# Kernel tuning notes

Measured on AMD Instinct MI355X. Metric: run time of the kernel, lower is better.

The kernel has to match this reference:

```python
import jax, jax.numpy as jnp
import numpy as np

N = 50000
E = 800000
IN_C, HID, LAT = 256, 128, 64


def setup_inputs() -> dict:
    key = jax.random.key(0)
    ks = jax.random.split(key, 8)
    x = jax.random.normal(ks[0], (N, IN_C), dtype=jnp.float32)
    edge_index = jax.random.randint(ks[1], (2, E), 0, N, dtype=jnp.int64)
    # Glorot-ish scaled weights (PyG GCNConv: Linear weight + separate bias)
    W1 = jax.random.normal(ks[2], (IN_C, HID), dtype=jnp.float32) / np.sqrt(IN_C)
    b1 = jnp.zeros((HID,), dtype=jnp.float32)
    Wmu = jax.random.normal(ks[3], (HID, LAT), dtype=jnp.float32) / np.sqrt(HID)
    bmu = jnp.zeros((LAT,), dtype=jnp.float32)
    Wlv = jax.random.normal(ks[4], (HID, LAT), dtype=jnp.float32) / np.sqrt(HID)
    blv = jnp.zeros((LAT,), dtype=jnp.float32)
    return {"x": x, "edge_index": edge_index, "W1": W1, "b1": b1,
            "Wmu": Wmu, "bmu": bmu, "Wlv": Wlv, "blv": blv}


def gcn_conv(x, edge_index, W, b):
    """PyG GCNConv: add self-loops, sym-normalize, transform, scatter-add."""
    n = x.shape[0]
    loop = jnp.arange(n, dtype=edge_index.dtype)
    row = jnp.concatenate([edge_index[0], loop])  # source
    col = jnp.concatenate([edge_index[1], loop])  # target
    deg = jax.ops.segment_sum(jnp.ones_like(col, dtype=x.dtype), col, num_segments=n)
    dinv = jax.lax.rsqrt(jnp.maximum(deg, 1e-12))  # deg >= 1 due to self-loops
    norm = dinv[row] * dinv[col]                   # [E+N]
    h = x @ W                                      # transform first (smaller width)
    msg = h[row] * norm[:, None]                   # [E+N, out] gathered messages
    out = jax.ops.segment_sum(msg, col, num_segments=n)
    return out + b


def reference(x, edge_index, W1, b1, Wmu, bmu, Wlv, blv):
    h = jax.nn.relu(gcn_conv(x, edge_index, W1, b1))
    # dropout p=0.0 -> identity
    mu = gcn_conv(h, edge_index, Wmu, bmu)
    logvar = gcn_conv(h, edge_index, Wlv, blv)
    return (mu, logvar)
```

## Files before the change

### kernel.cpp

```cpp
#include <hip/hip_runtime.h>
#include <stdint.h>

#define NN   50000
#define NE   800000
#define INC  256
#define HID  128
#define LAT  64

typedef unsigned short u16;
typedef short v8s __attribute__((ext_vector_type(8)));
typedef float v4f __attribute__((ext_vector_type(4)));

#define SLAB_OFF 0
#define OFFS_OFF 802816
#define W1P_OFF  881216
#define W2P_OFF  897600
#define G1_OFF   905792

#define NBIN        196
#define OFFS_STRIDE 200
#define NSLAB       784

#define G2_OFFU  8388608
#define C2_CNT   8388608
#define C2_DINV  8438608
#define C2_BKT   8488608

#define GB    782

__device__ __forceinline__ u16 f2b(float f) {
    union { float f; uint32_t i; } c; c.f = f;
    uint32_t r = c.i + 0x7FFF + ((c.i >> 16) & 1);
    return (u16)(r >> 16);
}
__device__ __forceinline__ float blo(unsigned u) { return __uint_as_float(u << 16); }
__device__ __forceinline__ float bhi(unsigned u) { return __uint_as_float(u & 0xffff0000u); }

__device__ void pack1_body(const float* __restrict__ W1, u16* __restrict__ W1P, int b) {
    int tg = b * 256 + threadIdx.x;
    int ks = tg >> 9, rem = tg & 511;
    int nt = rem >> 6, lane = rem & 63;
    int quad = lane >> 4, l15 = lane & 15;
    u16 o[8];
    #pragma unroll
    for (int j = 0; j < 8; j++)
        o[j] = f2b(W1[(long)(ks * 32 + quad * 8 + j) * HID + nt * 16 + l15]);
    *(ushort4*)(W1P + (long)tg * 8)     = make_ushort4(o[0], o[1], o[2], o[3]);
    *(ushort4*)(W1P + (long)tg * 8 + 4) = make_ushort4(o[4], o[5], o[6], o[7]);
}

__device__ void pack2_body(const float* __restrict__ Wmu, const float* __restrict__ Wlv,
                           u16* __restrict__ W2P, int b) {
    int tg = b * 256 + threadIdx.x;
    int ks = tg >> 9, rem = tg & 511;
    int nt = rem >> 6, lane = rem & 63;
    int quad = lane >> 4, l15 = lane & 15;
    const float* W = (nt < 4) ? Wmu : Wlv;
    int ntl = (nt < 4) ? nt : nt - 4;
    u16 o[8];
    #pragma unroll
    for (int j = 0; j < 8; j++)
        o[j] = f2b(W[(long)(ks * 32 + quad * 8 + j) * LAT + ntl * 16 + l15]);
    *(ushort4*)(W2P + (long)tg * 8)     = make_ushort4(o[0], o[1], o[2], o[3]);
    *(ushort4*)(W2P + (long)tg * 8 + 4) = make_ushort4(o[4], o[5], o[6], o[7]);
}

__global__ __launch_bounds__(256) void k_fusedA(unsigned* csr, const float* W1,
        const float* Wmu, const float* Wlv) {
    int b = blockIdx.x;
    if (b < 16) pack1_body(W1, (u16*)(csr + W1P_OFF), b);
    else pack2_body(Wmu, Wlv, (u16*)(csr + W2P_OFF), b - 16);
}

__device__ void gemm1_body(const float* __restrict__ xbuf,
        const unsigned* __restrict__ csr, u16* __restrict__ g1, int blk) {
    const u16* W1P = (const u16*)(csr + W1P_OFF);
    int tid = threadIdx.x;
    int lane = tid & 63, w = tid >> 6;
    int quad = lane >> 4, l15 = lane & 15;
    int m0 = blk * 64 + w * 16;
    int arow = m0 + l15;
    int arc = arow < NN ? arow : NN - 1;
    const float* ap = xbuf + (long)arc * INC + quad * 8;
    const v8s* bp = (const v8s*)W1P;
    v4f acc[8];
    #pragma unroll
    for (int t = 0; t < 8; t++) acc[t] = (v4f){0.f, 0.f, 0.f, 0.f};

    float4 A[16];
    #pragma unroll
    for (int ks = 0; ks < 8; ks++) {
        A[2 * ks]     = *(const float4*)(ap + ks * 32);
        A[2 * ks + 1] = *(const float4*)(ap + ks * 32 + 4);
    }
    #pragma unroll
    for (int ks = 0; ks < 8; ks++) {
        float4 a0 = A[2 * ks], a1 = A[2 * ks + 1];
        v8s af;
        af[0] = (short)f2b(a0.x); af[1] = (short)f2b(a0.y);
        af[2] = (short)f2b(a0.z); af[3] = (short)f2b(a0.w);
        af[4] = (short)f2b(a1.x); af[5] = (short)f2b(a1.y);
        af[6] = (short)f2b(a1.z); af[7] = (short)f2b(a1.w);
        #pragma unroll
        for (int t = 0; t < 8; t++) {
            v8s bf = bp[(ks * 8 + t) * 64 + lane];
            acc[t] = __builtin_amdgcn_mfma_f32_16x16x32_bf16(af, bf, acc[t], 0, 0, 0);
        }
    }
    #pragma unroll
    for (int r = 0; r < 4; r++) {
        int rr = m0 + quad * 4 + r;
        if (rr < NN) {
            u16* dst = g1 + (long)rr * HID + l15;
            #pragma unroll
            for (int t = 0; t < 8; t++) dst[t * 16] = f2b(acc[t][r]);
        }
    }
}

__device__ void part_body(const int* __restrict__ row, const int* __restrict__ col,
                          unsigned* __restrict__ csr, int id) {
    __shared__ int hist[256];
    __shared__ int scanbuf[256];
    __shared__ unsigned recs[1024];
    int tid = threadIdx.x;
    int base = id * 1024;
    hist[tid] = 0;
    __syncthreads();
    int v[4], u[4];
    #pragma unroll
    for (int i = 0; i < 4; i++) {
        int e = base + i * 256 + tid;
        if (e < NE) {
            v[i] = col[e]; u[i] = row[e];
            atomicAdd(&hist[v[i] >> 8], 1);
        } else v[i] = -1;
    }
    __syncthreads();
    int x = hist[tid];
    scanbuf[tid] = x;
    __syncthreads();
    for (int s = 1; s < 256; s <<= 1) {
        int y = (tid >= s) ? scanbuf[tid - s] : 0;
        __syncthreads();
        scanbuf[tid] += y;
        __syncthreads();
    }
    int excl = scanbuf[tid] - x;
    u16* offs = (u16*)(csr + OFFS_OFF) + (long)id * OFFS_STRIDE;
    if (tid <= NBIN) offs[tid] = (u16)excl;
    hist[tid] = excl;
    __syncthreads();
    #pragma unroll
    for (int i = 0; i < 4; i++) {
        if (v[i] >= 0) {
            int slot = atomicAdd(&hist[v[i] >> 8], 1);
            recs[slot] = (unsigned)u[i] | ((unsigned)(v[i] & 255) << 16);
        }
    }
    __syncthreads();
    unsigned* slab = csr + SLAB_OFF + (long)id * 1024;
    #pragma unroll
    for (int i = 0; i < 4; i++) slab[i * 256 + tid] = recs[i * 256 + tid];
}

__global__ __launch_bounds__(256) void k_fusedB(const float* __restrict__ xbuf,
        unsigned* __restrict__ csr, u16* __restrict__ g1,
        const int* __restrict__ row, const int* __restrict__ col) {
    int b = blockIdx.x;
    if (b < GB) gemm1_body(xbuf, csr, g1, b);
    part_body(row, col, csr, b);
}

__global__ __launch_bounds__(256) void k_merge(const unsigned* __restrict__ csr,
        unsigned* __restrict__ xb) {
    __shared__ int cnt_lds[256];
    __shared__ u16 bkt_lds[256 * 64];
    int tid = threadIdx.x;
    int bin = blockIdx.x;
    cnt_lds[tid] = 0;
    __syncthreads();
    const u16* offs = (const u16*)(csr + OFFS_OFF);
    const unsigned* slab = csr + SLAB_OFF;
    for (int s = tid; s < NSLAB; s += 256) {
        int st = offs[s * OFFS_STRIDE + bin];
        int en = offs[s * OFFS_STRIDE + bin + 1];
        for (int j = st; j < en; j++) {
            unsigned r = slab[s * 1024 + j];
            int vlo = (int)(r >> 16);
            int slot = atomicAdd(&cnt_lds[vlo], 1);
            if (slot < 64) bkt_lds[(vlo << 6) + slot] = (u16)(r & 0xffffu);
        }
    }
    __syncthreads();
    int* cnt2 = (int*)(xb + C2_CNT);
    float* dinv = (float*)(xb + C2_DINV);
    u16* bkt2 = (u16*)(xb + C2_BKT);
    int v0 = bin << 8;
    {
        int v = v0 + tid;
        if (v < NN) {
            int deg = cnt_lds[tid];
            int cn = deg < 64 ? deg : 64;
            cnt2[v] = cn;
            dinv[v] = rsqrtf((float)(deg + 1));
        }
    }
    const uint4* src = (const uint4*)bkt_lds;
    #pragma unroll
    for (int i = 0; i < 8; i++) {
        int idx = i * 256 + tid;
        int node = idx >> 3;
        if (v0 + node < NN)
            ((uint4*)(bkt2 + ((long)(v0 + node) << 6)))[idx & 7] = src[idx];
    }
}

#define ACC8(P, D, W) if (P) { \
    a0 += D * blo(W.x); a1 += D * bhi(W.x); a2 += D * blo(W.y); a3 += D * bhi(W.y); \
    a4 += D * blo(W.z); a5 += D * bhi(W.z); a6 += D * blo(W.w); a7 += D * bhi(W.w); }
#define RED(S) \
    a0 += __shfl_xor(a0, S); a1 += __shfl_xor(a1, S); a2 += __shfl_xor(a2, S); \
    a3 += __shfl_xor(a3, S); a4 += __shfl_xor(a4, S); a5 += __shfl_xor(a5, S); \
    a6 += __shfl_xor(a6, S); a7 += __shfl_xor(a7, S);

#define GATHER_LOOP(SRC) \
    for (int t = 0; t < cn; t += 32) { \
        int t0 = t + q, t1 = t0 + 4, t2 = t0 + 8,  t3 = t0 + 12, \
            t4 = t0 + 16, t5 = t0 + 20, t6 = t0 + 24, t7 = t0 + 28; \
        bool p0 = t0 < cn, p1 = t1 < cn, p2 = t2 < cn, p3 = t3 < cn, \
             p4 = t4 < cn, p5 = t5 < cn, p6 = t6 < cn, p7 = t7 < cn; \
        int u0 = __shfl(idx, t0), u1 = __shfl(idx, t1), u2 = __shfl(idx, t2), \
            u3 = __shfl(idx, t3), u4 = __shfl(idx, t4), u5 = __shfl(idx, t5), \
            u6 = __shfl(idx, t6), u7 = __shfl(idx, t7); \
        float d0 = __shfl(dvu, t0), d1 = __shfl(dvu, t1), d2 = __shfl(dvu, t2), \
              d3 = __shfl(dvu, t3), d4 = __shfl(dvu, t4), d5 = __shfl(dvu, t5), \
              d6 = __shfl(dvu, t6), d7 = __shfl(dvu, t7); \
        uint4 w0, w1, w2, w3, w4, w5, w6, w7; \
        if (p0) w0 = *(const uint4*)(SRC + (long)u0 * HID + c * 8); \
        if (p1) w1 = *(const uint4*)(SRC + (long)u1 * HID + c * 8); \
        if (p2) w2 = *(const uint4*)(SRC + (long)u2 * HID + c * 8); \
        if (p3) w3 = *(const uint4*)(SRC + (long)u3 * HID + c * 8); \
        if (p4) w4 = *(const uint4*)(SRC + (long)u4 * HID + c * 8); \
        if (p5) w5 = *(const uint4*)(SRC + (long)u5 * HID + c * 8); \
        if (p6) w6 = *(const uint4*)(SRC + (long)u6 * HID + c * 8); \
        if (p7) w7 = *(const uint4*)(SRC + (long)u7 * HID + c * 8); \
        ACC8(p0, d0, w0) \
        ACC8(p1, d1, w1) \
        ACC8(p2, d2, w2) \
        ACC8(p3, d3, w3) \
        ACC8(p4, d4, w4) \
        ACC8(p5, d5, w5) \
        ACC8(p6, d6, w6) \
        ACC8(p7, d7, w7) \
    }

__global__ __launch_bounds__(256) void k_gather1(const u16* __restrict__ g1,
        const unsigned* __restrict__ xb, const float* __restrict__ b1,
        u16* __restrict__ h) {
    int tid = threadIdx.x;
    int lane = tid & 63, w = tid >> 6;
    int v = blockIdx.x * 4 + w;
    int q = lane >> 4, c = lane & 15;
    const int* cnt2 = (const int*)(xb + C2_CNT);
    const float* dinv = (const float*)(xb + C2_DINV);
    const u16* bkt2 = (const u16*)(xb + C2_BKT);
    int cn = cnt2[v];
    float dvv = dinv[v];
    int idx = (lane < cn) ? (int)bkt2[(v << 6) + lane] : 0;
    float dvu = dinv[idx];
    float a0 = 0.f, a1 = 0.f, a2 = 0.f, a3 = 0.f, a4 = 0.f, a5 = 0.f, a6 = 0.f, a7 = 0.f;
    if (q == 0) {
        uint4 wv = *(const uint4*)(g1 + (long)v * HID + c * 8);
        a0 = dvv * blo(wv.x); a1 = dvv * bhi(wv.x); a2 = dvv * blo(wv.y); a3 = dvv * bhi(wv.y);
        a4 = dvv * blo(wv.z); a5 = dvv * bhi(wv.z); a6 = dvv * blo(wv.w); a7 = dvv * bhi(wv.w);
    }
    GATHER_LOOP(g1)
    RED(16)
    RED(32)
    if (q == 0) {
        int j = c * 8;
        float r[8] = {a0, a1, a2, a3, a4, a5, a6, a7};
        unsigned p[4];
        #pragma unroll
        for (int i = 0; i < 4; i++) {
            float x0 = dvv * r[2 * i]     + b1[j + 2 * i];
            float x1 = dvv * r[2 * i + 1] + b1[j + 2 * i + 1];
            x0 = x0 > 0.f ? x0 : 0.f;
            x1 = x1 > 0.f ? x1 : 0.f;
            p[i] = (unsigned)f2b(x0) | ((unsigned)f2b(x1) << 16);
        }
        uint4 o; o.x = p[0]; o.y = p[1]; o.z = p[2]; o.w = p[3];
        *(uint4*)(h + (long)v * HID + j) = o;
    }
}

__global__ __launch_bounds__(256) void k_gemm2(const u16* __restrict__ h,
        const unsigned* __restrict__ csr, u16* __restrict__ g2) {
    const u16* W2P = (const u16*)(csr + W2P_OFF);
    int tid = threadIdx.x;
    int lane = tid & 63, w = tid >> 6;
    int quad = lane >> 4, l15 = lane & 15;
    int m0 = blockIdx.x * 64 + w * 16;
    int arow = m0 + l15;
    int arc = arow < NN ? arow : NN - 1;
    const u16* ap = h + (long)arc * HID + quad * 8;
    const v8s* bp = (const v8s*)W2P;
    v4f acc[8];
    #pragma unroll
    for (int t = 0; t < 8; t++) acc[t] = (v4f){0.f, 0.f, 0.f, 0.f};

    v8s af[4];
    #pragma unroll
    for (int ks = 0; ks < 4; ks++) af[ks] = *(const v8s*)(ap + ks * 32);

    #pragma unroll
    for (int ks = 0; ks < 4; ks++) {
        #pragma unroll
        for (int t = 0; t < 8; t++) {
            v8s bf = bp[(ks * 8 + t) * 64 + lane];
            acc[t] = __builtin_amdgcn_mfma_f32_16x16x32_bf16(af[ks], bf, acc[t], 0, 0, 0);
        }
    }
    #pragma unroll
    for (int r = 0; r < 4; r++) {
        int rr = m0 + quad * 4 + r;
        if (rr < NN) {
            u16* dst = g2 + (long)rr * HID + l15;
            #pragma unroll
            for (int t = 0; t < 8; t++) dst[t * 16] = f2b(acc[t][r]);
        }
    }
}

__global__ __launch_bounds__(256) void k_gather2(const u16* __restrict__ g2,
        const unsigned* __restrict__ xb, const float* __restrict__ bmu,
        const float* __restrict__ blv, float* __restrict__ out) {
    int tid = threadIdx.x;
    int lane = tid & 63, w = tid >> 6;
    int v = blockIdx.x * 4 + w;
    int q = lane >> 4, c = lane & 15;
    const int* cnt2 = (const int*)(xb + C2_CNT);
    const float* dinv = (const float*)(xb + C2_DINV);
    const u16* bkt2 = (const u16*)(xb + C2_BKT);
    int cn = cnt2[v];
    float dvv = dinv[v];
    int idx = (lane < cn) ? (int)bkt2[(v << 6) + lane] : 0;
    float dvu = dinv[idx];
    float a0 = 0.f, a1 = 0.f, a2 = 0.f, a3 = 0.f, a4 = 0.f, a5 = 0.f, a6 = 0.f, a7 = 0.f;
    if (q == 0) {
        uint4 wv = *(const uint4*)(g2 + (long)v * HID + c * 8);
        a0 = dvv * blo(wv.x); a1 = dvv * bhi(wv.x); a2 = dvv * blo(wv.y); a3 = dvv * bhi(wv.y);
        a4 = dvv * blo(wv.z); a5 = dvv * bhi(wv.z); a6 = dvv * blo(wv.w); a7 = dvv * bhi(wv.w);
    }
    GATHER_LOOP(g2)
    RED(16)
    RED(32)
    if (q == 0) {
        float r[8] = {a0, a1, a2, a3, a4, a5, a6, a7};
        if (c < 8) {
            int j = c * 8;
            float4 o0 = make_float4(dvv * r[0] + bmu[j],     dvv * r[1] + bmu[j + 1],
                                    dvv * r[2] + bmu[j + 2], dvv * r[3] + bmu[j + 3]);
            float4 o1 = make_float4(dvv * r[4] + bmu[j + 4], dvv * r[5] + bmu[j + 5],
                                    dvv * r[6] + bmu[j + 6], dvv * r[7] + bmu[j + 7]);
            float* dst = out + (long)v * LAT + j;
            *(float4*)dst = o0;
            *(float4*)(dst + 4) = o1;
        } else {
            int j = c * 8 - 64;
            float4 o0 = make_float4(dvv * r[0] + blv[j],     dvv * r[1] + blv[j + 1],
                                    dvv * r[2] + blv[j + 2], dvv * r[3] + blv[j + 3]);
            float4 o1 = make_float4(dvv * r[4] + blv[j + 4], dvv * r[5] + blv[j + 5],
                                    dvv * r[6] + blv[j + 6], dvv * r[7] + blv[j + 7]);
            float* dst = out + (long)NN * LAT + (long)v * LAT + j;
            *(float4*)dst = o0;
            *(float4*)(dst + 4) = o1;
        }
    }
}

extern "C" void kernel_launch(void* const* d_in, const int* in_sizes, int n_in,
                              void* d_out, int out_size, void* d_ws, size_t ws_size,
                              hipStream_t stream) {
    float* xbuf = (float*)d_in[0];
    const int* ei  = (const int*)d_in[1];
    const float* W1  = (const float*)d_in[2];
    const float* b1  = (const float*)d_in[3];
    const float* Wmu = (const float*)d_in[4];
    const float* bmu = (const float*)d_in[5];
    const float* Wlv = (const float*)d_in[6];
    const float* blv = (const float*)d_in[7];
    const int* row = ei;
    const int* col = ei + NE;

    unsigned* csr = (unsigned*)d_out;
    u16* g1   = (u16*)(csr + G1_OFF);
    u16* hbuf = (u16*)xbuf;
    u16* g2   = (u16*)xbuf + G2_OFFU;
    unsigned* xb = (unsigned*)xbuf;

    k_fusedA<<<24, 256, 0, stream>>>(csr, W1, Wmu, Wlv);

    k_fusedB<<<NSLAB, 256, 0, stream>>>(xbuf, csr, g1, row, col);
    k_merge <<<NBIN, 256, 0, stream>>>(csr, xb);
    k_gather1<<<NN / 4, 256, 0, stream>>>(g1, xb, b1, hbuf);

    k_gemm2 <<<GB, 256, 0, stream>>>(hbuf, csr, g2);
    k_gather2<<<NN / 4, 256, 0, stream>>>(g2, xb, bmu, blv, (float*)d_out);
}
```

Measured before the change: 223.1 us.

## Split gather features into 32-column slabs and stage GEMM1 A tile in LDS

The g1, h and g2 intermediates move from row-major [N,128] to four column slabs of [N,32], and each gather kernel launches four times as many blocks, one feature slice per block. The aim is a smaller per-pass working set so neighbour rows gathered at random stay in cache. The cost is that every block reloads the neighbour index and degree data four times and issues narrower 4-byte loads. GEMM1 also converts its x tile to bf16 once into padded LDS before the MFMA loop, replacing the per-lane register staging.

```diff
diff --git a/kernel.cpp b/kernel.cpp
--- a/kernel.cpp
+++ b/kernel.cpp
@@ -27,6 +27,7 @@
 #define C2_BKT   8488608
 
 #define GB    782
+#define GPB   12500
 
 __device__ __forceinline__ u16 f2b(float f) {
     union { float f; uint32_t i; } c; c.f = f;
@@ -73,34 +74,31 @@
 }
 
 __device__ void gemm1_body(const float* __restrict__ xbuf,
-        const unsigned* __restrict__ csr, u16* __restrict__ g1, int blk) {
+        const unsigned* __restrict__ csr, u16* __restrict__ g1, int blk,
+        u16* __restrict__ As) {
     const u16* W1P = (const u16*)(csr + W1P_OFF);
     int tid = threadIdx.x;
+    int m0b = blk * 64;
+    #pragma unroll
+    for (int i = 0; i < 16; i++) {
+        int idx = i * 256 + tid;
+        int r = idx >> 6, c4 = idx & 63;
+        int gr = m0b + r; gr = gr < NN ? gr : NN - 1;
+        float4 a = *(const float4*)(xbuf + (long)gr * INC + c4 * 4);
+        *(ushort4*)(As + r * 264 + c4 * 4) =
+            make_ushort4(f2b(a.x), f2b(a.y), f2b(a.z), f2b(a.w));
+    }
+    __syncthreads();
     int lane = tid & 63, w = tid >> 6;
     int quad = lane >> 4, l15 = lane & 15;
-    int m0 = blk * 64 + w * 16;
-    int arow = m0 + l15;
-    int arc = arow < NN ? arow : NN - 1;
-    const float* ap = xbuf + (long)arc * INC + quad * 8;
+    int m0 = m0b + w * 16;
     const v8s* bp = (const v8s*)W1P;
     v4f acc[8];
     #pragma unroll
     for (int t = 0; t < 8; t++) acc[t] = (v4f){0.f, 0.f, 0.f, 0.f};
-
-    float4 A[16];
     #pragma unroll
     for (int ks = 0; ks < 8; ks++) {
-        A[2 * ks]     = *(const float4*)(ap + ks * 32);
-        A[2 * ks + 1] = *(const float4*)(ap + ks * 32 + 4);
-    }
-    #pragma unroll
-    for (int ks = 0; ks < 8; ks++) {
-        float4 a0 = A[2 * ks], a1 = A[2 * ks + 1];
-        v8s af;
-        af[0] = (short)f2b(a0.x); af[1] = (short)f2b(a0.y);
-        af[2] = (short)f2b(a0.z); af[3] = (short)f2b(a0.w);
-        af[4] = (short)f2b(a1.x); af[5] = (short)f2b(a1.y);
-        af[6] = (short)f2b(a1.z); af[7] = (short)f2b(a1.w);
+        v8s af = *(const v8s*)(As + (w * 16 + l15) * 264 + ks * 32 + quad * 8);
         #pragma unroll
         for (int t = 0; t < 8; t++) {
             v8s bf = bp[(ks * 8 + t) * 64 + lane];
@@ -111,18 +109,16 @@
     for (int r = 0; r < 4; r++) {
         int rr = m0 + quad * 4 + r;
         if (rr < NN) {
-            u16* dst = g1 + (long)rr * HID + l15;
             #pragma unroll
-            for (int t = 0; t < 8; t++) dst[t * 16] = f2b(acc[t][r]);
+            for (int t = 0; t < 8; t++)
+                g1[((long)(t >> 1) * NN + rr) * 32 + (t & 1) * 16 + l15] = f2b(acc[t][r]);
         }
     }
 }
 
 __device__ void part_body(const int* __restrict__ row, const int* __restrict__ col,
-                          unsigned* __restrict__ csr, int id) {
-    __shared__ int hist[256];
-    __shared__ int scanbuf[256];
-    __shared__ unsigned recs[1024];
+                          unsigned* __restrict__ csr, int id,
+                          int* hist, int* scanbuf, unsigned* recs) {
     int tid = threadIdx.x;
     int base = id * 1024;
     hist[tid] = 0;
@@ -167,9 +163,13 @@
 __global__ __launch_bounds__(256) void k_fusedB(const float* __restrict__ xbuf,
         unsigned* __restrict__ csr, u16* __restrict__ g1,
         const int* __restrict__ row, const int* __restrict__ col) {
+    __shared__ __align__(16) u16 As[64 * 264];
+    __shared__ int hist[256];
+    __shared__ int scanbuf[256];
+    __shared__ unsigned recs[1024];
     int b = blockIdx.x;
-    if (b < GB) gemm1_body(xbuf, csr, g1, b);
-    part_body(row, col, csr, b);
+    if (b < GB) gemm1_body(xbuf, csr, g1, b, As);
+    part_body(row, col, csr, b, hist, scanbuf, recs);
 }
 
 __global__ __launch_bounds__(256) void k_merge(const unsigned* __restrict__ csr,
@@ -216,15 +216,8 @@
     }
 }
 
-#define ACC8(P, D, W) if (P) { \
-    a0 += D * blo(W.x); a1 += D * bhi(W.x); a2 += D * blo(W.y); a3 += D * bhi(W.y); \
-    a4 += D * blo(W.z); a5 += D * bhi(W.z); a6 += D * blo(W.w); a7 += D * bhi(W.w); }
-#define RED(S) \
-    a0 += __shfl_xor(a0, S); a1 += __shfl_xor(a1, S); a2 += __shfl_xor(a2, S); \
-    a3 += __shfl_xor(a3, S); a4 += __shfl_xor(a4, S); a5 += __shfl_xor(a5, S); \
-    a6 += __shfl_xor(a6, S); a7 += __shfl_xor(a7, S);
-
-#define GATHER_LOOP(SRC) \
+#define GACC(P, D, W) if (P) { a0 += D * blo(W); a1 += D * bhi(W); }
+#define GATHER_SLICE_LOOP(GS) \
     for (int t = 0; t < cn; t += 32) { \
         int t0 = t + q, t1 = t0 + 4, t2 = t0 + 8,  t3 = t0 + 12, \
             t4 = t0 + 16, t5 = t0 + 20, t6 = t0 + 24, t7 = t0 + 28; \
@@ -236,31 +229,36 @@
         float d0 = __shfl(dvu, t0), d1 = __shfl(dvu, t1), d2 = __shfl(dvu, t2), \
               d3 = __shfl(dvu, t3), d4 = __shfl(dvu, t4), d5 = __shfl(dvu, t5), \
               d6 = __shfl(dvu, t6), d7 = __shfl(dvu, t7); \
-        uint4 w0, w1, w2, w3, w4, w5, w6, w7; \
-        if (p0) w0 = *(const uint4*)(SRC + (long)u0 * HID + c * 8); \
-        if (p1) w1 = *(const uint4*)(SRC + (long)u1 * HID + c * 8); \
-        if (p2) w2 = *(const uint4*)(SRC + (long)u2 * HID + c * 8); \
-        if (p3) w3 = *(const uint4*)(SRC + (long)u3 * HID + c * 8); \
-        if (p4) w4 = *(const uint4*)(SRC + (long)u4 * HID + c * 8); \
-        if (p5) w5 = *(const uint4*)(SRC + (long)u5 * HID + c * 8); \
-        if (p6) w6 = *(const uint4*)(SRC + (long)u6 * HID + c * 8); \
-        if (p7) w7 = *(const uint4*)(SRC + (long)u7 * HID + c * 8); \
-        ACC8(p0, d0, w0) \
-        ACC8(p1, d1, w1) \
-        ACC8(p2, d2, w2) \
-        ACC8(p3, d3, w3) \
-        ACC8(p4, d4, w4) \
-        ACC8(p5, d5, w5) \
-        ACC8(p6, d6, w6) \
-        ACC8(p7, d7, w7) \
-    }
+        unsigned w0 = 0, w1 = 0, w2 = 0, w3 = 0, w4 = 0, w5 = 0, w6 = 0, w7 = 0; \
+        if (p0) w0 = *(const unsigned*)(GS + (long)u0 * 32 + c * 2); \
+        if (p1) w1 = *(const unsigned*)(GS + (long)u1 * 32 + c * 2); \
+        if (p2) w2 = *(const unsigned*)(GS + (long)u2 * 32 + c * 2); \
+        if (p3) w3 = *(const unsigned*)(GS + (long)u3 * 32 + c * 2); \
+        if (p4) w4 = *(const unsigned*)(GS + (long)u4 * 32 + c * 2); \
+        if (p5) w5 = *(const unsigned*)(GS + (long)u5 * 32 + c * 2); \
+        if (p6) w6 = *(const unsigned*)(GS + (long)u6 * 32 + c * 2); \
+        if (p7) w7 = *(const unsigned*)(GS + (long)u7 * 32 + c * 2); \
+        GACC(p0, d0, w0) \
+        GACC(p1, d1, w1) \
+        GACC(p2, d2, w2) \
+        GACC(p3, d3, w3) \
+        GACC(p4, d4, w4) \
+        GACC(p5, d5, w5) \
+        GACC(p6, d6, w6) \
+        GACC(p7, d7, w7) \
+    }
+#define GRED() \
+    a0 += __shfl_xor(a0, 16); a1 += __shfl_xor(a1, 16); \
+    a0 += __shfl_xor(a0, 32); a1 += __shfl_xor(a1, 32);
 
 __global__ __launch_bounds__(256) void k_gather1(const u16* __restrict__ g1,
         const unsigned* __restrict__ xb, const float* __restrict__ b1,
         u16* __restrict__ h) {
     int tid = threadIdx.x;
     int lane = tid & 63, w = tid >> 6;
-    int v = blockIdx.x * 4 + w;
+    int bid = blockIdx.x;
+    int p = bid / GPB;
+    int v = (bid - p * GPB) * 4 + w;
     int q = lane >> 4, c = lane & 15;
     const int* cnt2 = (const int*)(xb + C2_CNT);
     const float* dinv = (const float*)(xb + C2_DINV);
@@ -269,29 +267,22 @@
     float dvv = dinv[v];
     int idx = (lane < cn) ? (int)bkt2[(v << 6) + lane] : 0;
     float dvu = dinv[idx];
-    float a0 = 0.f, a1 = 0.f, a2 = 0.f, a3 = 0.f, a4 = 0.f, a5 = 0.f, a6 = 0.f, a7 = 0.f;
+    const u16* gs = g1 + (long)p * NN * 32;
+    float a0 = 0.f, a1 = 0.f;
     if (q == 0) {
-        uint4 wv = *(const uint4*)(g1 + (long)v * HID + c * 8);
-        a0 = dvv * blo(wv.x); a1 = dvv * bhi(wv.x); a2 = dvv * blo(wv.y); a3 = dvv * bhi(wv.y);
-        a4 = dvv * blo(wv.z); a5 = dvv * bhi(wv.z); a6 = dvv * blo(wv.w); a7 = dvv * bhi(wv.w);
-    }
-    GATHER_LOOP(g1)
-    RED(16)
-    RED(32)
+        unsigned wv = *(const unsigned*)(gs + (long)v * 32 + c * 2);
+        a0 = dvv * blo(wv); a1 = dvv * bhi(wv);
+    }
+    GATHER_SLICE_LOOP(gs)
+    GRED()
     if (q == 0) {
-        int j = c * 8;
-        float r[8] = {a0, a1, a2, a3, a4, a5, a6, a7};
-        unsigned p[4];
-        #pragma unroll
-        for (int i = 0; i < 4; i++) {
-            float x0 = dvv * r[2 * i]     + b1[j + 2 * i];
-            float x1 = dvv * r[2 * i + 1] + b1[j + 2 * i + 1];
-            x0 = x0 > 0.f ? x0 : 0.f;
-            x1 = x1 > 0.f ? x1 : 0.f;
-            p[i] = (unsigned)f2b(x0) | ((unsigned)f2b(x1) << 16);
-        }
-        uint4 o; o.x = p[0]; o.y = p[1]; o.z = p[2]; o.w = p[3];
-        *(uint4*)(h + (long)v * HID + j) = o;
+        int j = p * 32 + c * 2;
+        float x0 = dvv * a0 + b1[j];
+        float x1 = dvv * a1 + b1[j + 1];
+        x0 = x0 > 0.f ? x0 : 0.f;
+        x1 = x1 > 0.f ? x1 : 0.f;
+        *(unsigned*)(h + ((long)p * NN + v) * 32 + c * 2) =
+            (unsigned)f2b(x0) | ((unsigned)f2b(x1) << 16);
     }
 }
 
@@ -304,7 +295,6 @@
     int m0 = blockIdx.x * 64 + w * 16;
     int arow = m0 + l15;
     int arc = arow < NN ? arow : NN - 1;
-    const u16* ap = h + (long)arc * HID + quad * 8;
     const v8s* bp = (const v8s*)W2P;
     v4f acc[8];
     #pragma unroll
@@ -312,7 +302,8 @@
 
     v8s af[4];
     #pragma unroll
-    for (int ks = 0; ks < 4; ks++) af[ks] = *(const v8s*)(ap + ks * 32);
+    for (int ks = 0; ks < 4; ks++)
+        af[ks] = *(const v8s*)(h + ((long)ks * NN + arc) * 32 + quad * 8);
 
     #pragma unroll
     for (int ks = 0; ks < 4; ks++) {
@@ -326,9 +317,9 @@
     for (int r = 0; r < 4; r++) {
         int rr = m0 + quad * 4 + r;
         if (rr < NN) {
-            u16* dst = g2 + (long)rr * HID + l15;
             #pragma unroll
-            for (int t = 0; t < 8; t++) dst[t * 16] = f2b(acc[t][r]);
+            for (int t = 0; t < 8; t++)
+                g2[((long)(t >> 1) * NN + rr) * 32 + (t & 1) * 16 + l15] = f2b(acc[t][r]);
         }
     }
 }
@@ -338,7 +329,9 @@
         const float* __restrict__ blv, float* __restrict__ out) {
     int tid = threadIdx.x;
     int lane = tid & 63, w = tid >> 6;
-    int v = blockIdx.x * 4 + w;
+    int bid = blockIdx.x;
+    int p = bid / GPB;
+    int v = (bid - p * GPB) * 4 + w;
     int q = lane >> 4, c = lane & 15;
     const int* cnt2 = (const int*)(xb + C2_CNT);
     const float* dinv = (const float*)(xb + C2_DINV);
@@ -347,35 +340,23 @@
     float dvv = dinv[v];
     int idx = (lane < cn) ? (int)bkt2[(v << 6) + lane] : 0;
     float dvu = dinv[idx];
-    float a0 = 0.f, a1 = 0.f, a2 = 0.f, a3 = 0.f, a4 = 0.f, a5 = 0.f, a6 = 0.f, a7 = 0.f;
+    const u16* gs = g2 + (long)p * NN * 32;
+    float a0 = 0.f, a1 = 0.f;
     if (q == 0) {
-        uint4 wv = *(const uint4*)(g2 + (long)v * HID + c * 8);
-        a0 = dvv * blo(wv.x); a1 = dvv * bhi(wv.x); a2 = dvv * blo(wv.y); a3 = dvv * bhi(wv.y);
-        a4 = dvv * blo(wv.z); a5 = dvv * bhi(wv.z); a6 = dvv * blo(wv.w); a7 = dvv * bhi(wv.w);
-    }
-    GATHER_LOOP(g2)
-    RED(16)
-    RED(32)
+        unsigned wv = *(const unsigned*)(gs + (long)v * 32 + c * 2);
+        a0 = dvv * blo(wv); a1 = dvv * bhi(wv);
+    }
+    GATHER_SLICE_LOOP(gs)
+    GRED()
     if (q == 0) {
-        float r[8] = {a0, a1, a2, a3, a4, a5, a6, a7};
-        if (c < 8) {
-            int j = c * 8;
-            float4 o0 = make_float4(dvv * r[0] + bmu[j],     dvv * r[1] + bmu[j + 1],
-                                    dvv * r[2] + bmu[j + 2], dvv * r[3] + bmu[j + 3]);
-            float4 o1 = make_float4(dvv * r[4] + bmu[j + 4], dvv * r[5] + bmu[j + 5],
-                                    dvv * r[6] + bmu[j + 6], dvv * r[7] + bmu[j + 7]);
-            float* dst = out + (long)v * LAT + j;
-            *(float4*)dst = o0;
-            *(float4*)(dst + 4) = o1;
+        int j = p * 32 + c * 2;
+        if (j < 64) {
+            *(float2*)(out + (long)v * LAT + j) =
+                make_float2(dvv * a0 + bmu[j], dvv * a1 + bmu[j + 1]);
         } else {
-            int j = c * 8 - 64;
-            float4 o0 = make_float4(dvv * r[0] + blv[j],     dvv * r[1] + blv[j + 1],
-                                    dvv * r[2] + blv[j + 2], dvv * r[3] + blv[j + 3]);
-            float4 o1 = make_float4(dvv * r[4] + blv[j + 4], dvv * r[5] + blv[j + 5],
-                                    dvv * r[6] + blv[j + 6], dvv * r[7] + blv[j + 7]);
-            float* dst = out + (long)NN * LAT + (long)v * LAT + j;
-            *(float4*)dst = o0;
-            *(float4*)(dst + 4) = o1;
+            int jl = j - 64;
+            *(float2*)(out + (long)NN * LAT + (long)v * LAT + jl) =
+                make_float2(dvv * a0 + blv[jl], dvv * a1 + blv[jl + 1]);
         }
     }
 }
@@ -404,8 +385,8 @@
 
     k_fusedB<<<NSLAB, 256, 0, stream>>>(xbuf, csr, g1, row, col);
     k_merge <<<NBIN, 256, 0, stream>>>(csr, xb);
-    k_gather1<<<NN / 4, 256, 0, stream>>>(g1, xb, b1, hbuf);
+    k_gather1<<<4 * GPB, 256, 0, stream>>>(g1, xb, b1, hbuf);
 
     k_gemm2 <<<GB, 256, 0, stream>>>(hbuf, csr, g2);
-    k_gather2<<<NN / 4, 256, 0, stream>>>(g2, xb, bmu, blv, (float*)d_out);
-}
+    k_gather2<<<4 * GPB, 256, 0, stream>>>(g2, xb, bmu, blv, (float*)d_out);
+}
```

Result: slower. 280.0 us (+25.5%).

## Fuse layer-1 gather with second GEMM via LDS and stage GEMM1 A tile in LDS

Applied to the files above, without the earlier changes.

Merges the layer-1 aggregation kernel with the second GEMM. Each 64-row block now aggregates its own nodes into an LDS tile of ReLU'd bf16 features and runs the MFMA transform straight from LDS, so the h round-trip through global memory and one launch go away. The first GEMM also now stages its A tile in padded LDS using coalesced float4 loads, instead of each lane loading strided rows itself. The trade-off is that the fused kernel runs only GB blocks, about 782, with each wave handling 16 nodes serially, so gather parallelism and latency hiding drop. The extra LDS in k_fusedB may also cut occupancy for the partition work.

```diff
diff --git a/kernel.cpp b/kernel.cpp
--- a/kernel.cpp
+++ b/kernel.cpp
@@ -73,34 +73,31 @@
 }
 
 __device__ void gemm1_body(const float* __restrict__ xbuf,
-        const unsigned* __restrict__ csr, u16* __restrict__ g1, int blk) {
+        const unsigned* __restrict__ csr, u16* __restrict__ g1, int blk,
+        u16* __restrict__ As) {
     const u16* W1P = (const u16*)(csr + W1P_OFF);
     int tid = threadIdx.x;
+    int m0b = blk * 64;
+    #pragma unroll
+    for (int i = 0; i < 16; i++) {
+        int idx = i * 256 + tid;
+        int r = idx >> 6, c4 = idx & 63;
+        int gr = m0b + r; gr = gr < NN ? gr : NN - 1;
+        float4 a = *(const float4*)(xbuf + (long)gr * INC + c4 * 4);
+        *(ushort4*)(As + r * 264 + c4 * 4) =
+            make_ushort4(f2b(a.x), f2b(a.y), f2b(a.z), f2b(a.w));
+    }
+    __syncthreads();
     int lane = tid & 63, w = tid >> 6;
     int quad = lane >> 4, l15 = lane & 15;
-    int m0 = blk * 64 + w * 16;
-    int arow = m0 + l15;
-    int arc = arow < NN ? arow : NN - 1;
-    const float* ap = xbuf + (long)arc * INC + quad * 8;
+    int m0 = m0b + w * 16;
     const v8s* bp = (const v8s*)W1P;
     v4f acc[8];
     #pragma unroll
     for (int t = 0; t < 8; t++) acc[t] = (v4f){0.f, 0.f, 0.f, 0.f};
-
-    float4 A[16];
     #pragma unroll
     for (int ks = 0; ks < 8; ks++) {
-        A[2 * ks]     = *(const float4*)(ap + ks * 32);
-        A[2 * ks + 1] = *(const float4*)(ap + ks * 32 + 4);
-    }
-    #pragma unroll
-    for (int ks = 0; ks < 8; ks++) {
-        float4 a0 = A[2 * ks], a1 = A[2 * ks + 1];
-        v8s af;
-        af[0] = (short)f2b(a0.x); af[1] = (short)f2b(a0.y);
-        af[2] = (short)f2b(a0.z); af[3] = (short)f2b(a0.w);
-        af[4] = (short)f2b(a1.x); af[5] = (short)f2b(a1.y);
-        af[6] = (short)f2b(a1.z); af[7] = (short)f2b(a1.w);
+        v8s af = *(const v8s*)(As + (w * 16 + l15) * 264 + ks * 32 + quad * 8);
         #pragma unroll
         for (int t = 0; t < 8; t++) {
             v8s bf = bp[(ks * 8 + t) * 64 + lane];
@@ -119,10 +116,8 @@
 }
 
 __device__ void part_body(const int* __restrict__ row, const int* __restrict__ col,
-                          unsigned* __restrict__ csr, int id) {
-    __shared__ int hist[256];
-    __shared__ int scanbuf[256];
-    __shared__ unsigned recs[1024];
+                          unsigned* __restrict__ csr, int id,
+                          int* hist, int* scanbuf, unsigned* recs) {
     int tid = threadIdx.x;
     int base = id * 1024;
     hist[tid] = 0;
@@ -167,9 +162,13 @@
 __global__ __launch_bounds__(256) void k_fusedB(const float* __restrict__ xbuf,
         unsigned* __restrict__ csr, u16* __restrict__ g1,
         const int* __restrict__ row, const int* __restrict__ col) {
+    __shared__ __align__(16) u16 As[64 * 264];
+    __shared__ int hist[256];
+    __shared__ int scanbuf[256];
+    __shared__ unsigned recs[1024];
     int b = blockIdx.x;
-    if (b < GB) gemm1_body(xbuf, csr, g1, b);
-    part_body(row, col, csr, b);
+    if (b < GB) gemm1_body(xbuf, csr, g1, b, As);
+    part_body(row, col, csr, b, hist, scanbuf, recs);
 }
 
 __global__ __launch_bounds__(256) void k_merge(const unsigned* __restrict__ csr,
@@ -223,7 +222,6 @@
     a0 += __shfl_xor(a0, S); a1 += __shfl_xor(a1, S); a2 += __shfl_xor(a2, S); \
     a3 += __shfl_xor(a3, S); a4 += __shfl_xor(a4, S); a5 += __shfl_xor(a5, S); \
     a6 += __shfl_xor(a6, S); a7 += __shfl_xor(a7, S);
-
 #define GATHER_LOOP(SRC) \
     for (int t = 0; t < cn; t += 32) { \
         int t0 = t + q, t1 = t0 + 4, t2 = t0 + 8,  t3 = t0 + 12, \
@@ -255,71 +253,73 @@
         ACC8(p7, d7, w7) \
     }
 
-__global__ __launch_bounds__(256) void k_gather1(const u16* __restrict__ g1,
+#define HPAD 136
+__global__ __launch_bounds__(256) void k_fusedD(const u16* __restrict__ g1,
         const unsigned* __restrict__ xb, const float* __restrict__ b1,
-        u16* __restrict__ h) {
+        const unsigned* __restrict__ csr, u16* __restrict__ g2) {
+    __shared__ __align__(16) u16 hs[64 * HPAD];
     int tid = threadIdx.x;
     int lane = tid & 63, w = tid >> 6;
-    int v = blockIdx.x * 4 + w;
     int q = lane >> 4, c = lane & 15;
     const int* cnt2 = (const int*)(xb + C2_CNT);
     const float* dinv = (const float*)(xb + C2_DINV);
     const u16* bkt2 = (const u16*)(xb + C2_BKT);
-    int cn = cnt2[v];
-    float dvv = dinv[v];
-    int idx = (lane < cn) ? (int)bkt2[(v << 6) + lane] : 0;
-    float dvu = dinv[idx];
-    float a0 = 0.f, a1 = 0.f, a2 = 0.f, a3 = 0.f, a4 = 0.f, a5 = 0.f, a6 = 0.f, a7 = 0.f;
-    if (q == 0) {
-        uint4 wv = *(const uint4*)(g1 + (long)v * HID + c * 8);
-        a0 = dvv * blo(wv.x); a1 = dvv * bhi(wv.x); a2 = dvv * blo(wv.y); a3 = dvv * bhi(wv.y);
-        a4 = dvv * blo(wv.z); a5 = dvv * bhi(wv.z); a6 = dvv * blo(wv.w); a7 = dvv * bhi(wv.w);
-    }
-    GATHER_LOOP(g1)
-    RED(16)
-    RED(32)
-    if (q == 0) {
-        int j = c * 8;
-        float r[8] = {a0, a1, a2, a3, a4, a5, a6, a7};
-        unsigned p[4];
-        #pragma unroll
-        for (int i = 0; i < 4; i++) {
-            float x0 = dvv * r[2 * i]     + b1[j + 2 * i];
-            float x1 = dvv * r[2 * i + 1] + b1[j + 2 * i + 1];
-            x0 = x0 > 0.f ? x0 : 0.f;
-            x1 = x1 > 0.f ? x1 : 0.f;
-            p[i] = (unsigned)f2b(x0) | ((unsigned)f2b(x1) << 16);
-        }
-        uint4 o; o.x = p[0]; o.y = p[1]; o.z = p[2]; o.w = p[3];
-        *(uint4*)(h + (long)v * HID + j) = o;
-    }
-}
-
-__global__ __launch_bounds__(256) void k_gemm2(const u16* __restrict__ h,
-        const unsigned* __restrict__ csr, u16* __restrict__ g2) {
+    int m0b = blockIdx.x * 64;
+
+    #pragma unroll 1
+    for (int n = 0; n < 16; n++) {
+        int v = m0b + w * 16 + n;
+        int vc = v < NN ? v : NN - 1;
+        int cn = cnt2[vc];
+        float dvv = dinv[vc];
+        int idx = (lane < cn) ? (int)bkt2[((long)vc << 6) + lane] : 0;
+        float dvu = dinv[idx];
+        float a0 = 0.f, a1 = 0.f, a2 = 0.f, a3 = 0.f,
+              a4 = 0.f, a5 = 0.f, a6 = 0.f, a7 = 0.f;
+        if (q == 0) {
+            uint4 wv = *(const uint4*)(g1 + (long)vc * HID + c * 8);
+            a0 = dvv * blo(wv.x); a1 = dvv * bhi(wv.x);
+            a2 = dvv * blo(wv.y); a3 = dvv * bhi(wv.y);
+            a4 = dvv * blo(wv.z); a5 = dvv * bhi(wv.z);
+            a6 = dvv * blo(wv.w); a7 = dvv * bhi(wv.w);
+        }
+        GATHER_LOOP(g1)
+        RED(16)
+        RED(32)
+        if (q == 0) {
+            int j = c * 8;
+            float r[8] = {a0, a1, a2, a3, a4, a5, a6, a7};
+            unsigned p[4];
+            #pragma unroll
+            for (int i = 0; i < 4; i++) {
+                float x0 = dvv * r[2 * i]     + b1[j + 2 * i];
+                float x1 = dvv * r[2 * i + 1] + b1[j + 2 * i + 1];
+                x0 = x0 > 0.f ? x0 : 0.f;
+                x1 = x1 > 0.f ? x1 : 0.f;
+                p[i] = (unsigned)f2b(x0) | ((unsigned)f2b(x1) << 16);
+            }
+            *(ushort4*)(hs + (w * 16 + n) * HPAD + j) =
+                make_ushort4((u16)p[0], (u16)(p[0] >> 16), (u16)p[1], (u16)(p[1] >> 16));
+            *(ushort4*)(hs + (w * 16 + n) * HPAD + j + 4) =
+                make_ushort4((u16)p[2], (u16)(p[2] >> 16), (u16)p[3], (u16)(p[3] >> 16));
+        }
+    }
+    __syncthreads();
+
     const u16* W2P = (const u16*)(csr + W2P_OFF);
-    int tid = threadIdx.x;
-    int lane = tid & 63, w = tid >> 6;
     int quad = lane >> 4, l15 = lane & 15;
-    int m0 = blockIdx.x * 64 + w * 16;
-    int arow = m0 + l15;
-    int arc = arow < NN ? arow : NN - 1;
-    const u16* ap = h + (long)arc * HID + quad * 8;
+    int m0 = m0b + w * 16;
     const v8s* bp = (const v8s*)W2P;
     v4f acc[8];
     #pragma unroll
     for (int t = 0; t < 8; t++) acc[t] = (v4f){0.f, 0.f, 0.f, 0.f};
-
-    v8s af[4];
-    #pragma unroll
-    for (int ks = 0; ks < 4; ks++) af[ks] = *(const v8s*)(ap + ks * 32);
-
     #pragma unroll
     for (int ks = 0; ks < 4; ks++) {
+        v8s af = *(const v8s*)(hs + (w * 16 + l15) * HPAD + ks * 32 + quad * 8);
         #pragma unroll
         for (int t = 0; t < 8; t++) {
             v8s bf = bp[(ks * 8 + t) * 64 + lane];
-            acc[t] = __builtin_amdgcn_mfma_f32_16x16x32_bf16(af[ks], bf, acc[t], 0, 0, 0);
+            acc[t] = __builtin_amdgcn_mfma_f32_16x16x32_bf16(af, bf, acc[t], 0, 0, 0);
         }
     }
     #pragma unroll
@@ -345,7 +345,7 @@
     const u16* bkt2 = (const u16*)(xb + C2_BKT);
     int cn = cnt2[v];
     float dvv = dinv[v];
-    int idx = (lane < cn) ? (int)bkt2[(v << 6) + lane] : 0;
+    int idx = (lane < cn) ? (int)bkt2[((long)v << 6) + lane] : 0;
     float dvu = dinv[idx];
     float a0 = 0.f, a1 = 0.f, a2 = 0.f, a3 = 0.f, a4 = 0.f, a5 = 0.f, a6 = 0.f, a7 = 0.f;
     if (q == 0) {
@@ -396,7 +396,6 @@
 
     unsigned* csr = (unsigned*)d_out;
     u16* g1   = (u16*)(csr + G1_OFF);
-    u16* hbuf = (u16*)xbuf;
     u16* g2   = (u16*)xbuf + G2_OFFU;
     unsigned* xb = (unsigned*)xbuf;
 
@@ -404,8 +403,8 @@
 
     k_fusedB<<<NSLAB, 256, 0, stream>>>(xbuf, csr, g1, row, col);
     k_merge <<<NBIN, 256, 0, stream>>>(csr, xb);
-    k_gather1<<<NN / 4, 256, 0, stream>>>(g1, xb, b1, hbuf);
-
-    k_gemm2 <<<GB, 256, 0, stream>>>(hbuf, csr, g2);
+
+    k_fusedD<<<GB, 256, 0, stream>>>(g1, xb, b1, csr, g2);
+
     k_gather2<<<NN / 4, 256, 0, stream>>>(g2, xb, bmu, blv, (float*)d_out);
 }
```

After: 220.3 us. Within noise of the previous version (-1.3%).
